# Optimization experiments

Measured on AMD Instinct MI355X. Metric: run time of the kernel, lower is better.

Reference implementation:

```python
import jax, jax.numpy as jnp
import numpy as np

NUM_FEATURES = 1_000_000
EMB_DIM = 16
NUM_FIELDS = 39
CIN_SIZES = (200, 200, 200)
DNN_SIZES = (400, 400)


def setup_inputs() -> dict:
    key = jax.random.key(0)
    ks = jax.random.split(key, 16)
    B = 2048
    inp = {}
    inp["feature_ids"] = jax.random.randint(ks[0], (B, NUM_FIELDS), 0, NUM_FEATURES)
    inp["feature_vals"] = jax.random.uniform(ks[1], (B, NUM_FIELDS), dtype=jnp.float32)
    # embeddings (xavier-normal-ish scale)
    inp["emb"] = jax.random.normal(ks[2], (NUM_FEATURES, EMB_DIM), jnp.float32) * 0.02
    inp["bias_emb"] = jax.random.normal(ks[3], (NUM_FEATURES, 1), jnp.float32) * 0.02
    # CIN conv1d (kernel size 1) weights: (out, in)
    field_nums = [NUM_FIELDS]
    for i, size in enumerate(CIN_SIZES):
        cin_in = field_nums[-1] * NUM_FIELDS
        inp[f"cin_W{i}"] = jax.random.normal(ks[4 + i], (size, cin_in), jnp.float32) / np.sqrt(cin_in)
        inp[f"cin_b{i}"] = jnp.zeros((size,), jnp.float32)
        field_nums.append(size // 2 if i != len(CIN_SIZES) - 1 else size)
    # DNN linears: (out, in)
    last = NUM_FIELDS * EMB_DIM
    for i, size in enumerate(DNN_SIZES):
        inp[f"dnn_W{i}"] = jax.random.normal(ks[8 + i], (size, last), jnp.float32) / np.sqrt(last)
        inp[f"dnn_b{i}"] = jnp.zeros((size,), jnp.float32)
        last = size
    hidden_size = sum(CIN_SIZES[:-1]) // 2 + CIN_SIZES[-1]  # 400
    fc_in = hidden_size + DNN_SIZES[-1]
    inp["fc_W"] = jax.random.normal(ks[12], (1, fc_in), jnp.float32) / np.sqrt(fc_in)
    inp["fc_b"] = jnp.zeros((1,), jnp.float32)
    return inp


def _forward(feature_ids, feature_vals, emb, bias_emb,
             cin_W0, cin_b0, cin_W1, cin_b1, cin_W2, cin_b2,
             dnn_W0, dnn_b0, dnn_W1, dnn_b1, fc_W, fc_b):
    B = feature_ids.shape[0]
    inputs = emb[feature_ids] * feature_vals[:, :, None]        # [B, F, D]
    input_biases = bias_emb[feature_ids][..., 0] * feature_vals  # [B, F]

    # CIN
    Ws = (cin_W0, cin_W1, cin_W2)
    bs = (cin_b0, cin_b1, cin_b2)
    h = inputs
    finals = []
    n_layers = len(CIN_SIZES)
    for i in range(n_layers):
        size = CIN_SIZES[i]
        x = jnp.einsum('bhd,bmd->bhmd', h, inputs)              # [B, H, F, D]
        x = x.reshape(B, -1, EMB_DIM)                           # [B, H*F, D]
        x = jnp.einsum('bcd,oc->bod', x, Ws[i]) + bs[i][None, :, None]  # 1x1 conv
        x = jax.nn.relu(x)
        if i != n_layers - 1:
            h, direct = x[:, : size // 2], x[:, size // 2:]
        else:
            direct = x
        finals.append(direct)
    cin_result = jnp.sum(jnp.concatenate(finals, axis=1), axis=-1)  # [B, hidden]

    # DNN
    d = inputs.reshape(B, -1)
    d = jax.nn.relu(d @ dnn_W0.T + dnn_b0)
    d = jax.nn.relu(d @ dnn_W1.T + dnn_b1)

    out = (jnp.concatenate((cin_result, d), axis=1) @ fc_W.T + fc_b)[:, 0]
    return out + jnp.sum(input_biases, axis=1)                  # [B]


def reference(feature_ids, feature_vals, emb, bias_emb,
              cin_W0, cin_b0, cin_W1, cin_b1, cin_W2, cin_b2,
              dnn_W0, dnn_b0, dnn_W1, dnn_b1, fc_W, fc_b):
    return _forward(feature_ids, feature_vals, emb, bias_emb,
                    cin_W0, cin_b0, cin_W1, cin_b1, cin_W2, cin_b2,
                    dnn_W0, dnn_b0, dnn_W1, dnn_b1, fc_W, fc_b)
```

## Files before the change

kernel.cpp:

```cpp
#include <hip/hip_runtime.h>

#define B 2048
#define NF 39
#define D 16

typedef __bf16 bf16x8 __attribute__((ext_vector_type(8)));
typedef float f32x4 __attribute__((ext_vector_type(4)));

__device__ __forceinline__ void lds_barrier() {
  asm volatile("s_waitcnt lgkmcnt(0)" ::: "memory");
  __builtin_amdgcn_s_barrier();
}

__global__ __launch_bounds__(256) void gather_kernel(
    const int* __restrict__ fid, const float* __restrict__ fval,
    const float* __restrict__ emb, const float* __restrict__ bias_emb,
    float* __restrict__ inputs, float* __restrict__ biassum) {
  int b = blockIdx.x;
  __shared__ int ids[NF];
  __shared__ float vals[NF];
  int t = threadIdx.x;
  if (t < NF) { ids[t] = fid[b * NF + t]; vals[t] = fval[b * NF + t]; }
  __syncthreads();
  for (int i = t; i < NF * D; i += 256) {
    int f = i >> 4, d = i & 15;
    inputs[b * NF * D + i] = emb[(long)ids[f] * D + d] * vals[f];
  }
  if (t < 64) {
    float pb = (t < NF) ? bias_emb[ids[t]] * vals[t] : 0.f;
#pragma unroll
    for (int m = 32; m >= 1; m >>= 1) pb += __shfl_xor(pb, m);
    if (t == 0) biassum[b] = pb;
  }
}

__device__ __forceinline__ void prep_cin_one(const float* __restrict__ W,
                                             __bf16* __restrict__ Wg,
                                             int Hreal, int idx) {
  int l = idx & 63;
  int mt = (idx >> 6) % 13;
  int c = idx / (13 * 64);
  int o = mt * 16 + (l & 15);
  int kb = c * 32 + ((l >> 4) << 3);
  int rowlen = Hreal * 39;
  bf16x8 v;
#pragma unroll
  for (int j = 0; j < 8; ++j) {
    int k = kb + j;
    int h = k / 40;
    int m = k - h * 40;
    float val = 0.f;
    if (o < 200 && h < Hreal && m < 39) val = W[(long)o * rowlen + h * 39 + m];
    v[j] = (__bf16)val;
  }
  *reinterpret_cast<bf16x8*>(Wg + (long)idx * 8) = v;
}

__device__ __forceinline__ void prep_dnn_one(const float* __restrict__ W,
                                             __bf16* __restrict__ Wd,
                                             int IN, int idx) {
  int l = idx & 63;
  int tt = (idx >> 6) % 25;
  int c = idx / (25 * 64);
  int o = tt * 16 + (l & 15);
  int kb = c * 32 + ((l >> 4) << 3);
  bf16x8 v;
#pragma unroll
  for (int j = 0; j < 8; ++j) {
    int k = kb + j;
    v[j] = (k < IN) ? (__bf16)W[(long)o * IN + k] : (__bf16)0.f;
  }
  *reinterpret_cast<bf16x8*>(Wd + (long)idx * 8) = v;
}

#define PREP_T0 (52 * 13 * 64)
#define PREP_T12 (128 * 13 * 64)
#define PREP_T3 (20 * 25 * 64)
#define PREP_T4 (13 * 25 * 64)
#define PREP_TOTAL (PREP_T0 + 2 * PREP_T12 + PREP_T3 + PREP_T4)

__global__ void prep_all(const float* __restrict__ cW0, const float* __restrict__ cW1,
                         const float* __restrict__ cW2, const float* __restrict__ dW0,
                         const float* __restrict__ dW1, __bf16* __restrict__ Wg0,
                         __bf16* __restrict__ Wg1, __bf16* __restrict__ Wg2,
                         __bf16* __restrict__ Wd0, __bf16* __restrict__ Wd1) {
  int idx = blockIdx.x * 256 + threadIdx.x;
  if (idx < PREP_T0) { prep_cin_one(cW0, Wg0, 39, idx); return; }
  idx -= PREP_T0;
  if (idx < PREP_T12) { prep_cin_one(cW1, Wg1, 100, idx); return; }
  idx -= PREP_T12;
  if (idx < PREP_T12) { prep_cin_one(cW2, Wg2, 100, idx); return; }
  idx -= PREP_T12;
  if (idx < PREP_T3) { prep_dnn_one(dW0, Wd0, 624, idx); return; }
  idx -= PREP_T3;
  if (idx < PREP_T4) prep_dnn_one(dW1, Wd1, 400, idx);
}

__device__ __forceinline__ void form_x(const float* Hs, const float* Zs,
                                       __bf16* xbuf, int k0, int col) {
  int h = (int)((unsigned)k0 / 40u);
  int m0 = k0 - h * 40;
  float hv = Hs[h * 64 + col];
  const float4* zp = reinterpret_cast<const float4*>(Zs + col * 44 + m0);
  float4 za = zp[0], zb = zp[1];
  bf16x8 xv;
  xv[0] = (__bf16)(hv * za.x); xv[1] = (__bf16)(hv * za.y);
  xv[2] = (__bf16)(hv * za.z); xv[3] = (__bf16)(hv * za.w);
  xv[4] = (__bf16)(hv * zb.x); xv[5] = (__bf16)(hv * zb.y);
  xv[6] = (__bf16)(hv * zb.z); xv[7] = (__bf16)(hv * zb.w);
  int g = (k0 >> 3) & 15;
  *reinterpret_cast<bf16x8*>(
      reinterpret_cast<char*>(xbuf) + col * 256 + ((g * 16) ^ ((col & 7) << 4))) = xv;
}

template <int W, int NSTG, int SPLIT>
__device__ __forceinline__ void cin_layer(
    float* Hs, const float* Zs, __bf16* Xs,
    const __bf16* __restrict__ Wg, const float* __restrict__ bias,
    float* __restrict__ cin_out, int col_offset, int bbase, int t) {
  constexpr int TLO = (13 * W) >> 2;
  const int l = t & 63;
  const int q = l >> 4, dd = l & 15;
  const __bf16* wl = Wg + l * 8;

  f32x4 acc[13] = {};
  bf16x8 wf[16], wfn[16];
#pragma unroll
  for (int cc = 0; cc < 4; ++cc)
#pragma unroll
    for (int i = 0; i < 4; ++i)
      wf[cc * 4 + i] = *reinterpret_cast<const bf16x8*>(
          wl + (long)((cc * 13 + TLO + i) * 64) * 8);

#pragma unroll
  for (int j = 0; j < 4; ++j) form_x(Hs, Zs, Xs, (W + 4 * j) * 8, l);
  lds_barrier();

  for (int s = 0; s < NSTG; ++s) {
    __bf16* xcur = Xs + (s & 1) * 8192;
    __bf16* xnxt = Xs + ((s + 1) & 1) * 8192;
    const bool more = (s + 1 < NSTG);
    if (more) {
#pragma unroll
      for (int cc = 0; cc < 4; ++cc)
#pragma unroll
        for (int i = 0; i < 4; ++i)
          wfn[cc * 4 + i] = *reinterpret_cast<const bf16x8*>(
              wl + (long)((((s + 1) * 4 + cc) * 13 + TLO + i) * 64) * 8);
#pragma unroll
      for (int j = 0; j < 4; ++j)
        form_x(Hs, Zs, xnxt, (s + 1) * 128 + (W + 4 * j) * 8, l);
    }
#pragma unroll
    for (int cc = 0; cc < 4; ++cc) {
      bf16x8 bfr[4];
#pragma unroll
      for (int f = 0; f < 4; ++f) {
        int col = f * 16 + dd;
        int g = cc * 4 + q;
        bfr[f] = *reinterpret_cast<const bf16x8*>(
            reinterpret_cast<const char*>(xcur) + col * 256 +
            ((g * 16) ^ ((col & 7) << 4)));
      }
      __builtin_amdgcn_s_setprio(1);
#pragma unroll
      for (int i = 0; i < 13; ++i) {
        const int p = 13 * W + i;
        acc[i] = __builtin_amdgcn_mfma_f32_16x16x32_bf16(
            wf[cc * 4 + (p >> 2) - TLO], bfr[p & 3], acc[i], 0, 0, 0);
      }
      __builtin_amdgcn_s_setprio(0);
    }
    lds_barrier();
    if (more) {
#pragma unroll
      for (int i = 0; i < 16; ++i) wf[i] = wfn[i];
    }
  }

#pragma unroll
  for (int i = 0; i < 13; ++i) {
    const int p = 13 * W + i;
    const int tt = p >> 2, f = p & 3;
    const int b = bbase + f;
#pragma unroll
    for (int r = 0; r < 4; ++r) {
      int o = tt * 16 + q * 4 + r;
      if (o < 200) {
        float x = fmaxf(acc[i][r] + bias[o], 0.f);
        if (SPLIT && o < 100) {
          Hs[o * 64 + f * 16 + dd] = x;
        } else {
          x += __shfl_xor(x, 1);
          x += __shfl_xor(x, 2);
          x += __shfl_xor(x, 4);
          x += __shfl_xor(x, 8);
          if (dd == 0) cin_out[b * 400 + col_offset + o - (SPLIT ? 100 : 0)] = x;
        }
      }
    }
  }
  lds_barrier();
}

template <int W>
__device__ __forceinline__ void cin_all(
    float* Hs, const float* Zs, __bf16* Xs, const __bf16* Wg0,
    const __bf16* Wg1, const __bf16* Wg2, const float* cb0, const float* cb1,
    const float* cb2, float* cinres, int bbase, int t) {
  cin_layer<W, 13, 1>(Hs, Zs, Xs, Wg0, cb0, cinres, 0, bbase, t);
  cin_layer<W, 32, 1>(Hs, Zs, Xs, Wg1, cb1, cinres, 100, bbase, t);
  cin_layer<W, 32, 0>(Hs, Zs, Xs, Wg2, cb2, cinres, 200, bbase, t);
}

__global__ __launch_bounds__(256, 2) void cin_fused(
    const float* __restrict__ Zin, const __bf16* __restrict__ Wg0,
    const __bf16* __restrict__ Wg1, const __bf16* __restrict__ Wg2,
    const float* __restrict__ cb0, const float* __restrict__ cb1,
    const float* __restrict__ cb2, float* __restrict__ cinres) {
  __shared__ float Hs[103 * 64];
  __shared__ float Zs[64 * 44];
  __shared__ __bf16 Xs[2 * 8192];
  const int t = threadIdx.x;
  const int bbase = blockIdx.x * 4;

  for (int i = t; i < 64 * 44; i += 256) {
    int col = i / 44, m = i - (i / 44) * 44;
    int b = bbase + (col >> 4), d = col & 15;
    Zs[i] = (m < NF) ? Zin[((long)b * NF + m) * 16 + d] : 0.f;
  }
  for (int i = t; i < 103 * 64; i += 256) {
    int h = i >> 6, col = i & 63;
    int b = bbase + (col >> 4), d = col & 15;
    Hs[i] = (h < NF) ? Zin[((long)b * NF + h) * 16 + d] : 0.f;
  }
  __syncthreads();

  const int w = t >> 6;
  switch (w) {
    case 0: cin_all<0>(Hs, Zs, Xs, Wg0, Wg1, Wg2, cb0, cb1, cb2, cinres, bbase, t); break;
    case 1: cin_all<1>(Hs, Zs, Xs, Wg0, Wg1, Wg2, cb0, cb1, cb2, cinres, bbase, t); break;
    case 2: cin_all<2>(Hs, Zs, Xs, Wg0, Wg1, Wg2, cb0, cb1, cb2, cinres, bbase, t); break;
    default: cin_all<3>(Hs, Zs, Xs, Wg0, Wg1, Wg2, cb0, cb1, cb2, cinres, bbase, t); break;
  }
}

template <int IN>
__device__ __forceinline__ void dnn_stage_load(const float* __restrict__ x,
                                               int bg, int c, int t,
                                               float4& a, float4& b2) {
  int b = t >> 2, kb = t & 3;
  int k0 = c * 32 + kb * 8;
  if (k0 < IN) {
    const float4* p =
        reinterpret_cast<const float4*>(x + (long)(bg * 64 + b) * IN + k0);
    a = p[0];
    b2 = p[1];
  } else {
    a = make_float4(0.f, 0.f, 0.f, 0.f);
    b2 = make_float4(0.f, 0.f, 0.f, 0.f);
  }
}

__device__ __forceinline__ void dnn_stage_write(__bf16* Xs, int t, float4 a,
                                                float4 b2) {
  int b = t >> 2, kb = t & 3;
  bf16x8 v;
  v[0] = (__bf16)a.x;  v[1] = (__bf16)a.y;  v[2] = (__bf16)a.z;  v[3] = (__bf16)a.w;
  v[4] = (__bf16)b2.x; v[5] = (__bf16)b2.y; v[6] = (__bf16)b2.z; v[7] = (__bf16)b2.w;
  *reinterpret_cast<bf16x8*>(Xs + ((kb * 64 + b) << 3)) = v;
}

template <int W, int TG, int IN, int NCH>
__device__ __forceinline__ void dnn_core(
    const float* __restrict__ x, const __bf16* __restrict__ Wd,
    const float* __restrict__ bias, float* __restrict__ out, __bf16* Xs,
    int bg, int t) {
  constexpr int NT = (TG == 3) ? 7 : 6;
  constexpr int TGB = TG * 6;
  constexpr int PLO = NT * W;
  constexpr int TLO = PLO >> 2;
  constexpr int TN = ((PLO + NT - 1) >> 2) - TLO + 1;
  const int l = t & 63;
  const int q = l >> 4, dd = l & 15;
  const __bf16* wl = Wd + l * 8;

  f32x4 acc[NT] = {};
  bf16x8 wf[TN], wfn[TN];
#pragma unroll
  for (int i = 0; i < TN; ++i)
    wf[i] = *reinterpret_cast<const bf16x8*>(wl + (long)((TGB + TLO + i) * 64) * 8);

  float4 ra, rb;
  dnn_stage_load<IN>(x, bg, 0, t, ra, rb);
  dnn_stage_write(Xs, t, ra, rb);
  lds_barrier();

  for (int c = 0; c < NCH; ++c) {
    __bf16* cur = Xs + (c & 1) * 2048;
    __bf16* nxt = Xs + ((c + 1) & 1) * 2048;
    const bool more = (c + 1 < NCH);
    if (more) {
      dnn_stage_load<IN>(x, bg, c + 1, t, ra, rb);
#pragma unroll
      for (int i = 0; i < TN; ++i)
        wfn[i] = *reinterpret_cast<const bf16x8*>(
            wl + (long)(((c + 1) * 25 + TGB + TLO + i) * 64) * 8);
    }
    bf16x8 bfr[4];
#pragma unroll
    for (int f = 0; f < 4; ++f)
      bfr[f] = *reinterpret_cast<const bf16x8*>(cur + ((q * 64 + f * 16 + dd) << 3));
    __builtin_amdgcn_s_setprio(1);
#pragma unroll
    for (int i = 0; i < NT; ++i) {
      const int p = PLO + i;
      acc[i] = __builtin_amdgcn_mfma_f32_16x16x32_bf16(wf[(p >> 2) - TLO],
                                                       bfr[p & 3], acc[i], 0, 0, 0);
    }
    __builtin_amdgcn_s_setprio(0);
    if (more) dnn_stage_write(nxt, t, ra, rb);
    lds_barrier();
    if (more) {
#pragma unroll
      for (int i = 0; i < TN; ++i) wf[i] = wfn[i];
    }
  }

#pragma unroll
  for (int i = 0; i < NT; ++i) {
    const int p = PLO + i;
    const int gt = TGB + (p >> 2);
    const int f = p & 3;
    const int b = bg * 64 + f * 16 + dd;
#pragma unroll
    for (int r = 0; r < 4; ++r) {
      int o = gt * 16 + q * 4 + r;
      out[(long)b * 400 + o] = fmaxf(acc[i][r] + bias[o], 0.f);
    }
  }
}

template <int IN, int NCH>
__global__ __launch_bounds__(256) void dnn_mfma(
    const float* __restrict__ x, const __bf16* __restrict__ Wd,
    const float* __restrict__ bias, float* __restrict__ out) {
  __shared__ __bf16 Xs[2 * 4 * 64 * 8];
  const int blk = blockIdx.x;
  const int bg = blk >> 2, tg = blk & 3;
  const int t = threadIdx.x;
  const int w = t >> 6;
#define DNN_DISPATCH(TGV)                                                     \
  if (w == 0) dnn_core<0, TGV, IN, NCH>(x, Wd, bias, out, Xs, bg, t);         \
  else if (w == 1) dnn_core<1, TGV, IN, NCH>(x, Wd, bias, out, Xs, bg, t);    \
  else if (w == 2) dnn_core<2, TGV, IN, NCH>(x, Wd, bias, out, Xs, bg, t);    \
  else dnn_core<3, TGV, IN, NCH>(x, Wd, bias, out, Xs, bg, t);
  if (tg == 0) { DNN_DISPATCH(0) }
  else if (tg == 1) { DNN_DISPATCH(1) }
  else if (tg == 2) { DNN_DISPATCH(2) }
  else { DNN_DISPATCH(3) }
#undef DNN_DISPATCH
}

__global__ __launch_bounds__(256) void final_kernel(
    const float* __restrict__ cin, const float* __restrict__ d1,
    const float* __restrict__ fcW, const float* __restrict__ fcb,
    const float* __restrict__ biassum, float* __restrict__ out) {
  int b = blockIdx.x, t = threadIdx.x;
  float p = 0.f;
  for (int i = t; i < 800; i += 256) {
    float v = (i < 400) ? cin[b * 400 + i] : d1[b * 400 + (i - 400)];
    p += v * fcW[i];
  }
#pragma unroll
  for (int m = 32; m >= 1; m >>= 1) p += __shfl_xor(p, m);
  __shared__ float red[4];
  if ((t & 63) == 0) red[t >> 6] = p;
  __syncthreads();
  if (t == 0) out[b] = red[0] + red[1] + red[2] + red[3] + fcb[0] + biassum[b];
}

extern "C" void kernel_launch(void* const* d_in, const int* in_sizes, int n_in,
                              void* d_out, int out_size, void* d_ws,
                              size_t ws_size, hipStream_t stream) {
  (void)in_sizes; (void)n_in; (void)out_size; (void)ws_size;
  const int* fid = (const int*)d_in[0];
  const float* fval = (const float*)d_in[1];
  const float* emb = (const float*)d_in[2];
  const float* bias_emb = (const float*)d_in[3];
  const float* cW0 = (const float*)d_in[4];
  const float* cb0 = (const float*)d_in[5];
  const float* cW1 = (const float*)d_in[6];
  const float* cb1 = (const float*)d_in[7];
  const float* cW2 = (const float*)d_in[8];
  const float* cb2 = (const float*)d_in[9];
  const float* dW0 = (const float*)d_in[10];
  const float* db0 = (const float*)d_in[11];
  const float* dW1 = (const float*)d_in[12];
  const float* db1 = (const float*)d_in[13];
  const float* fcW = (const float*)d_in[14];
  const float* fcb = (const float*)d_in[15];
  float* out = (float*)d_out;

  float* ws = (float*)d_ws;
  float* inputs = ws;  ws += B * NF * D;
  float* biassum = ws; ws += B;
  float* cinres = ws;  ws += B * 400;
  float* dd0 = ws;     ws += B * 400;
  float* dd1 = ws;     ws += B * 400;
  __bf16* Wg0 = (__bf16*)ws; ws += (52 * 13 * 64 * 8) / 2;
  __bf16* Wg1 = (__bf16*)ws; ws += (128 * 13 * 64 * 8) / 2;
  __bf16* Wg2 = (__bf16*)ws; ws += (128 * 13 * 64 * 8) / 2;
  __bf16* Wd0 = (__bf16*)ws; ws += (20 * 25 * 64 * 8) / 2;
  __bf16* Wd1 = (__bf16*)ws; ws += (13 * 25 * 64 * 8) / 2;

  gather_kernel<<<B, 256, 0, stream>>>(fid, fval, emb, bias_emb, inputs, biassum);

  prep_all<<<(PREP_TOTAL + 255) / 256, 256, 0, stream>>>(
      cW0, cW1, cW2, dW0, dW1, Wg0, Wg1, Wg2, Wd0, Wd1);

  cin_fused<<<B / 4, 256, 0, stream>>>(inputs, Wg0, Wg1, Wg2, cb0, cb1, cb2, cinres);

  dnn_mfma<624, 20><<<128, 256, 0, stream>>>(inputs, Wd0, db0, dd0);
  dnn_mfma<400, 13><<<128, 256, 0, stream>>>(dd0, Wd1, db1, dd1);

  final_kernel<<<B, 256, 0, stream>>>(cinres, dd1, fcW, fcb, biassum, out);
}
```

Baseline: 207.1 us.

## Halve CIN batch tile per block and split DNN tiles across more blocks

The CIN kernel now handles 2 batch rows per block instead of 4, with a 64-wide K stage, smaller LDS buffers and a target of 4 blocks per CU, so twice as many blocks are launched with less LDS each. Each wave owns a contiguous range of output tiles and issues two MFMAs per stage. The DNN GEMMs are restructured so every block computes one 16-output tile for 64 rows, giving 800 blocks instead of 128. The aim is higher occupancy and more parallelism on the CUs, at the cost of more staging overhead per block, extra barriers, and reloading the activation tiles once for each output tile.

```diff
diff --git a/kernel.cpp b/kernel.cpp
--- a/kernel.cpp
+++ b/kernel.cpp
@@ -73,8 +73,8 @@
   *reinterpret_cast<bf16x8*>(Wd + (long)idx * 8) = v;
 }
 
-#define PREP_T0 (52 * 13 * 64)
-#define PREP_T12 (128 * 13 * 64)
+#define PREP_T0 (50 * 13 * 64)
+#define PREP_T12 (126 * 13 * 64)
 #define PREP_T3 (20 * 25 * 64)
 #define PREP_T4 (13 * 25 * 64)
 #define PREP_TOTAL (PREP_T0 + 2 * PREP_T12 + PREP_T3 + PREP_T4)
@@ -96,11 +96,11 @@
   if (idx < PREP_T4) prep_dnn_one(dW1, Wd1, 400, idx);
 }
 
-__device__ __forceinline__ void form_x(const float* Hs, const float* Zs,
-                                       __bf16* xbuf, int k0, int col) {
+__device__ __forceinline__ void form_x2(const float* Hs, const float* Zs,
+                                        __bf16* xbuf, int k0, int col) {
   int h = (int)((unsigned)k0 / 40u);
   int m0 = k0 - h * 40;
-  float hv = Hs[h * 64 + col];
+  float hv = Hs[h * 32 + col];
   const float4* zp = reinterpret_cast<const float4*>(Zs + col * 44 + m0);
   float4 za = zp[0], zb = zp[1];
   bf16x8 xv;
@@ -108,80 +108,87 @@
   xv[2] = (__bf16)(hv * za.z); xv[3] = (__bf16)(hv * za.w);
   xv[4] = (__bf16)(hv * zb.x); xv[5] = (__bf16)(hv * zb.y);
   xv[6] = (__bf16)(hv * zb.z); xv[7] = (__bf16)(hv * zb.w);
-  int g = (k0 >> 3) & 15;
+  int g = (k0 >> 3) & 7;
   *reinterpret_cast<bf16x8*>(
-      reinterpret_cast<char*>(xbuf) + col * 256 + ((g * 16) ^ ((col & 7) << 4))) = xv;
-}
-
-template <int W, int NSTG, int SPLIT>
-__device__ __forceinline__ void cin_layer(
+      reinterpret_cast<char*>(xbuf) + col * 128 + ((g * 16) ^ ((col & 7) << 4))) = xv;
+}
+
+template <int PLO, int NP, int NST, int SPLIT>
+__device__ __forceinline__ void cin_layer2(
     float* Hs, const float* Zs, __bf16* Xs,
     const __bf16* __restrict__ Wg, const float* __restrict__ bias,
     float* __restrict__ cin_out, int col_offset, int bbase, int t) {
-  constexpr int TLO = (13 * W) >> 2;
+  constexpr int TLO = PLO >> 1;
+  constexpr int THI = (PLO + NP - 1) >> 1;
+  constexpr int TN = THI - TLO + 1;
   const int l = t & 63;
   const int q = l >> 4, dd = l & 15;
+  const int xcol = t & 31;
+  const int xg = (t >> 5) & 7;
   const __bf16* wl = Wg + l * 8;
 
-  f32x4 acc[13] = {};
-  bf16x8 wf[16], wfn[16];
-#pragma unroll
-  for (int cc = 0; cc < 4; ++cc)
-#pragma unroll
-    for (int i = 0; i < 4; ++i)
-      wf[cc * 4 + i] = *reinterpret_cast<const bf16x8*>(
-          wl + (long)((cc * 13 + TLO + i) * 64) * 8);
-
-#pragma unroll
-  for (int j = 0; j < 4; ++j) form_x(Hs, Zs, Xs, (W + 4 * j) * 8, l);
+  f32x4 acc[NP] = {};
+  bf16x8 wf[TN][2], wfn[TN][2];
+#pragma unroll
+  for (int i = 0; i < TN; ++i)
+#pragma unroll
+    for (int c2 = 0; c2 < 2; ++c2)
+      wf[i][c2] = *reinterpret_cast<const bf16x8*>(
+          wl + (long)((c2 * 13 + TLO + i) * 64) * 8);
+
+  form_x2(Hs, Zs, Xs, xg * 8, xcol);
   lds_barrier();
 
-  for (int s = 0; s < NSTG; ++s) {
-    __bf16* xcur = Xs + (s & 1) * 8192;
-    __bf16* xnxt = Xs + ((s + 1) & 1) * 8192;
-    const bool more = (s + 1 < NSTG);
+  for (int s = 0; s < NST; ++s) {
+    __bf16* xcur = Xs + (s & 1) * 2048;
+    __bf16* xnxt = Xs + ((s + 1) & 1) * 2048;
+    const bool more = (s + 1 < NST);
     if (more) {
 #pragma unroll
-      for (int cc = 0; cc < 4; ++cc)
-#pragma unroll
-        for (int i = 0; i < 4; ++i)
-          wfn[cc * 4 + i] = *reinterpret_cast<const bf16x8*>(
-              wl + (long)((((s + 1) * 4 + cc) * 13 + TLO + i) * 64) * 8);
-#pragma unroll
-      for (int j = 0; j < 4; ++j)
-        form_x(Hs, Zs, xnxt, (s + 1) * 128 + (W + 4 * j) * 8, l);
-    }
-#pragma unroll
-    for (int cc = 0; cc < 4; ++cc) {
-      bf16x8 bfr[4];
-#pragma unroll
-      for (int f = 0; f < 4; ++f) {
+      for (int i = 0; i < TN; ++i)
+#pragma unroll
+        for (int c2 = 0; c2 < 2; ++c2)
+          wfn[i][c2] = *reinterpret_cast<const bf16x8*>(
+              wl + (long)((((s + 1) * 2 + c2) * 13 + TLO + i) * 64) * 8);
+    }
+    bf16x8 bfr[2][2];
+#pragma unroll
+    for (int f = 0; f < 2; ++f)
+#pragma unroll
+      for (int c2 = 0; c2 < 2; ++c2) {
         int col = f * 16 + dd;
-        int g = cc * 4 + q;
-        bfr[f] = *reinterpret_cast<const bf16x8*>(
-            reinterpret_cast<const char*>(xcur) + col * 256 +
+        int g = c2 * 4 + q;
+        bfr[f][c2] = *reinterpret_cast<const bf16x8*>(
+            reinterpret_cast<const char*>(xcur) + col * 128 +
             ((g * 16) ^ ((col & 7) << 4)));
       }
-      __builtin_amdgcn_s_setprio(1);
-#pragma unroll
-      for (int i = 0; i < 13; ++i) {
-        const int p = 13 * W + i;
-        acc[i] = __builtin_amdgcn_mfma_f32_16x16x32_bf16(
-            wf[cc * 4 + (p >> 2) - TLO], bfr[p & 3], acc[i], 0, 0, 0);
-      }
-      __builtin_amdgcn_s_setprio(0);
-    }
+    if (more) form_x2(Hs, Zs, xnxt, (s + 1) * 64 + xg * 8, xcol);
+    __builtin_amdgcn_s_setprio(1);
+#pragma unroll
+    for (int i = 0; i < NP; ++i) {
+      const int p = PLO + i;
+      const int ti = (p >> 1) - TLO;
+      const int f = p & 1;
+      acc[i] = __builtin_amdgcn_mfma_f32_16x16x32_bf16(wf[ti][0], bfr[f][0],
+                                                       acc[i], 0, 0, 0);
+      acc[i] = __builtin_amdgcn_mfma_f32_16x16x32_bf16(wf[ti][1], bfr[f][1],
+                                                       acc[i], 0, 0, 0);
+    }
+    __builtin_amdgcn_s_setprio(0);
     lds_barrier();
     if (more) {
 #pragma unroll
-      for (int i = 0; i < 16; ++i) wf[i] = wfn[i];
-    }
-  }
-
-#pragma unroll
-  for (int i = 0; i < 13; ++i) {
-    const int p = 13 * W + i;
-    const int tt = p >> 2, f = p & 3;
+      for (int i = 0; i < TN; ++i) {
+        wf[i][0] = wfn[i][0];
+        wf[i][1] = wfn[i][1];
+      }
+    }
+  }
+
+#pragma unroll
+  for (int i = 0; i < NP; ++i) {
+    const int p = PLO + i;
+    const int tt = p >> 1, f = p & 1;
     const int b = bbase + f;
 #pragma unroll
     for (int r = 0; r < 4; ++r) {
@@ -189,7 +196,7 @@
       if (o < 200) {
         float x = fmaxf(acc[i][r] + bias[o], 0.f);
         if (SPLIT && o < 100) {
-          Hs[o * 64 + f * 16 + dd] = x;
+          Hs[o * 32 + f * 16 + dd] = x;
         } else {
           x += __shfl_xor(x, 1);
           x += __shfl_xor(x, 2);
@@ -203,45 +210,46 @@
   lds_barrier();
 }
 
-template <int W>
-__device__ __forceinline__ void cin_all(
+template <int PLO, int NP>
+__device__ __forceinline__ void cin_all2(
     float* Hs, const float* Zs, __bf16* Xs, const __bf16* Wg0,
     const __bf16* Wg1, const __bf16* Wg2, const float* cb0, const float* cb1,
     const float* cb2, float* cinres, int bbase, int t) {
-  cin_layer<W, 13, 1>(Hs, Zs, Xs, Wg0, cb0, cinres, 0, bbase, t);
-  cin_layer<W, 32, 1>(Hs, Zs, Xs, Wg1, cb1, cinres, 100, bbase, t);
-  cin_layer<W, 32, 0>(Hs, Zs, Xs, Wg2, cb2, cinres, 200, bbase, t);
-}
-
-__global__ __launch_bounds__(256, 2) void cin_fused(
+  cin_layer2<PLO, NP, 25, 1>(Hs, Zs, Xs, Wg0, cb0, cinres, 0, bbase, t);
+  cin_layer2<PLO, NP, 63, 1>(Hs, Zs, Xs, Wg1, cb1, cinres, 100, bbase, t);
+  cin_layer2<PLO, NP, 63, 0>(Hs, Zs, Xs, Wg2, cb2, cinres, 200, bbase, t);
+}
+
+__global__ __launch_bounds__(256, 4) void cin_fused2(
     const float* __restrict__ Zin, const __bf16* __restrict__ Wg0,
     const __bf16* __restrict__ Wg1, const __bf16* __restrict__ Wg2,
     const float* __restrict__ cb0, const float* __restrict__ cb1,
     const float* __restrict__ cb2, float* __restrict__ cinres) {
-  __shared__ float Hs[103 * 64];
-  __shared__ float Zs[64 * 44];
-  __shared__ __bf16 Xs[2 * 8192];
+  __shared__ float Hs[101 * 32];
+  __shared__ float Zs[32 * 44];
+  __shared__ __bf16 Xs[2 * 2048];
   const int t = threadIdx.x;
-  const int bbase = blockIdx.x * 4;
-
-  for (int i = t; i < 64 * 44; i += 256) {
+  const int bbase = blockIdx.x * 2;
+
+  for (int i = t; i < 32 * 44; i += 256) {
     int col = i / 44, m = i - (i / 44) * 44;
     int b = bbase + (col >> 4), d = col & 15;
     Zs[i] = (m < NF) ? Zin[((long)b * NF + m) * 16 + d] : 0.f;
   }
-  for (int i = t; i < 103 * 64; i += 256) {
-    int h = i >> 6, col = i & 63;
+  for (int i = t; i < 41 * 32; i += 256) {
+    int h = i >> 5, col = i & 31;
     int b = bbase + (col >> 4), d = col & 15;
     Hs[i] = (h < NF) ? Zin[((long)b * NF + h) * 16 + d] : 0.f;
   }
+  if (t < 32) Hs[100 * 32 + t] = 0.f;
   __syncthreads();
 
   const int w = t >> 6;
   switch (w) {
-    case 0: cin_all<0>(Hs, Zs, Xs, Wg0, Wg1, Wg2, cb0, cb1, cb2, cinres, bbase, t); break;
-    case 1: cin_all<1>(Hs, Zs, Xs, Wg0, Wg1, Wg2, cb0, cb1, cb2, cinres, bbase, t); break;
-    case 2: cin_all<2>(Hs, Zs, Xs, Wg0, Wg1, Wg2, cb0, cb1, cb2, cinres, bbase, t); break;
-    default: cin_all<3>(Hs, Zs, Xs, Wg0, Wg1, Wg2, cb0, cb1, cb2, cinres, bbase, t); break;
+    case 0: cin_all2<0, 7>(Hs, Zs, Xs, Wg0, Wg1, Wg2, cb0, cb1, cb2, cinres, bbase, t); break;
+    case 1: cin_all2<7, 7>(Hs, Zs, Xs, Wg0, Wg1, Wg2, cb0, cb1, cb2, cinres, bbase, t); break;
+    case 2: cin_all2<14, 6>(Hs, Zs, Xs, Wg0, Wg1, Wg2, cb0, cb1, cb2, cinres, bbase, t); break;
+    default: cin_all2<20, 6>(Hs, Zs, Xs, Wg0, Wg1, Wg2, cb0, cb1, cb2, cinres, bbase, t); break;
   }
 }
 
@@ -271,25 +279,20 @@
   *reinterpret_cast<bf16x8*>(Xs + ((kb * 64 + b) << 3)) = v;
 }
 
-template <int W, int TG, int IN, int NCH>
-__device__ __forceinline__ void dnn_core(
+template <int IN, int NCH>
+__global__ __launch_bounds__(256) void dnn_mfma2(
     const float* __restrict__ x, const __bf16* __restrict__ Wd,
-    const float* __restrict__ bias, float* __restrict__ out, __bf16* Xs,
-    int bg, int t) {
-  constexpr int NT = (TG == 3) ? 7 : 6;
-  constexpr int TGB = TG * 6;
-  constexpr int PLO = NT * W;
-  constexpr int TLO = PLO >> 2;
-  constexpr int TN = ((PLO + NT - 1) >> 2) - TLO + 1;
-  const int l = t & 63;
+    const float* __restrict__ bias, float* __restrict__ out) {
+  __shared__ __bf16 Xs[2 * 2048];
+  const int bg = blockIdx.x / 25;
+  const int tile = blockIdx.x - bg * 25;
+  const int t = threadIdx.x;
+  const int w = t >> 6, l = t & 63;
   const int q = l >> 4, dd = l & 15;
   const __bf16* wl = Wd + l * 8;
 
-  f32x4 acc[NT] = {};
-  bf16x8 wf[TN], wfn[TN];
-#pragma unroll
-  for (int i = 0; i < TN; ++i)
-    wf[i] = *reinterpret_cast<const bf16x8*>(wl + (long)((TGB + TLO + i) * 64) * 8);
+  f32x4 acc = {};
+  bf16x8 wf = *reinterpret_cast<const bf16x8*>(wl + (long)(tile * 64) * 8);
 
   float4 ra, rb;
   dnn_stage_load<IN>(x, bg, 0, t, ra, rb);
@@ -300,66 +303,25 @@
     __bf16* cur = Xs + (c & 1) * 2048;
     __bf16* nxt = Xs + ((c + 1) & 1) * 2048;
     const bool more = (c + 1 < NCH);
+    bf16x8 wfn;
     if (more) {
       dnn_stage_load<IN>(x, bg, c + 1, t, ra, rb);
-#pragma unroll
-      for (int i = 0; i < TN; ++i)
-        wfn[i] = *reinterpret_cast<const bf16x8*>(
-            wl + (long)(((c + 1) * 25 + TGB + TLO + i) * 64) * 8);
-    }
-    bf16x8 bfr[4];
-#pragma unroll
-    for (int f = 0; f < 4; ++f)
-      bfr[f] = *reinterpret_cast<const bf16x8*>(cur + ((q * 64 + f * 16 + dd) << 3));
-    __builtin_amdgcn_s_setprio(1);
-#pragma unroll
-    for (int i = 0; i < NT; ++i) {
-      const int p = PLO + i;
-      acc[i] = __builtin_amdgcn_mfma_f32_16x16x32_bf16(wf[(p >> 2) - TLO],
-                                                       bfr[p & 3], acc[i], 0, 0, 0);
-    }
-    __builtin_amdgcn_s_setprio(0);
+      wfn = *reinterpret_cast<const bf16x8*>(
+          wl + (long)(((c + 1) * 25 + tile) * 64) * 8);
+    }
+    bf16x8 bfr = *reinterpret_cast<const bf16x8*>(cur + ((q * 64 + w * 16 + dd) << 3));
+    acc = __builtin_amdgcn_mfma_f32_16x16x32_bf16(wf, bfr, acc, 0, 0, 0);
     if (more) dnn_stage_write(nxt, t, ra, rb);
     lds_barrier();
-    if (more) {
-#pragma unroll
-      for (int i = 0; i < TN; ++i) wf[i] = wfn[i];
-    }
-  }
-
-#pragma unroll
-  for (int i = 0; i < NT; ++i) {
-    const int p = PLO + i;
-    const int gt = TGB + (p >> 2);
-    const int f = p & 3;
-    const int b = bg * 64 + f * 16 + dd;
-#pragma unroll
-    for (int r = 0; r < 4; ++r) {
-      int o = gt * 16 + q * 4 + r;
-      out[(long)b * 400 + o] = fmaxf(acc[i][r] + bias[o], 0.f);
-    }
-  }
-}
-
-template <int IN, int NCH>
-__global__ __launch_bounds__(256) void dnn_mfma(
-    const float* __restrict__ x, const __bf16* __restrict__ Wd,
-    const float* __restrict__ bias, float* __restrict__ out) {
-  __shared__ __bf16 Xs[2 * 4 * 64 * 8];
-  const int blk = blockIdx.x;
-  const int bg = blk >> 2, tg = blk & 3;
-  const int t = threadIdx.x;
-  const int w = t >> 6;
-#define DNN_DISPATCH(TGV)                                                     \
-  if (w == 0) dnn_core<0, TGV, IN, NCH>(x, Wd, bias, out, Xs, bg, t);         \
-  else if (w == 1) dnn_core<1, TGV, IN, NCH>(x, Wd, bias, out, Xs, bg, t);    \
-  else if (w == 2) dnn_core<2, TGV, IN, NCH>(x, Wd, bias, out, Xs, bg, t);    \
-  else dnn_core<3, TGV, IN, NCH>(x, Wd, bias, out, Xs, bg, t);
-  if (tg == 0) { DNN_DISPATCH(0) }
-  else if (tg == 1) { DNN_DISPATCH(1) }
-  else if (tg == 2) { DNN_DISPATCH(2) }
-  else { DNN_DISPATCH(3) }
-#undef DNN_DISPATCH
+    if (more) wf = wfn;
+  }
+
+  const int b = bg * 64 + w * 16 + dd;
+#pragma unroll
+  for (int r = 0; r < 4; ++r) {
+    int o = tile * 16 + q * 4 + r;
+    out[(long)b * 400 + o] = fmaxf(acc[r] + bias[o], 0.f);
+  }
 }
 
 __global__ __launch_bounds__(256) void final_kernel(
@@ -408,9 +370,9 @@
   float* cinres = ws;  ws += B * 400;
   float* dd0 = ws;     ws += B * 400;
   float* dd1 = ws;     ws += B * 400;
-  __bf16* Wg0 = (__bf16*)ws; ws += (52 * 13 * 64 * 8) / 2;
-  __bf16* Wg1 = (__bf16*)ws; ws += (128 * 13 * 64 * 8) / 2;
-  __bf16* Wg2 = (__bf16*)ws; ws += (128 * 13 * 64 * 8) / 2;
+  __bf16* Wg0 = (__bf16*)ws; ws += (50 * 13 * 64 * 8) / 2;
+  __bf16* Wg1 = (__bf16*)ws; ws += (126 * 13 * 64 * 8) / 2;
+  __bf16* Wg2 = (__bf16*)ws; ws += (126 * 13 * 64 * 8) / 2;
   __bf16* Wd0 = (__bf16*)ws; ws += (20 * 25 * 64 * 8) / 2;
   __bf16* Wd1 = (__bf16*)ws; ws += (13 * 25 * 64 * 8) / 2;
 
@@ -419,10 +381,10 @@
   prep_all<<<(PREP_TOTAL + 255) / 256, 256, 0, stream>>>(
       cW0, cW1, cW2, dW0, dW1, Wg0, Wg1, Wg2, Wd0, Wd1);
 
-  cin_fused<<<B / 4, 256, 0, stream>>>(inputs, Wg0, Wg1, Wg2, cb0, cb1, cb2, cinres);
-
-  dnn_mfma<624, 20><<<128, 256, 0, stream>>>(inputs, Wd0, db0, dd0);
-  dnn_mfma<400, 13><<<128, 256, 0, stream>>>(dd0, Wd1, db1, dd1);
+  cin_fused2<<<B / 2, 256, 0, stream>>>(inputs, Wg0, Wg1, Wg2, cb0, cb1, cb2, cinres);
+
+  dnn_mfma2<624, 20><<<32 * 25, 256, 0, stream>>>(inputs, Wd0, db0, dd0);
+  dnn_mfma2<400, 13><<<32 * 25, 256, 0, stream>>>(dd0, Wd1, db1, dd1);
 
   final_kernel<<<B, 256, 0, stream>>>(cinres, dd1, fcW, fcb, biassum, out);
 }
```

Measured after the change: 234.5 us. 1.13x slower.
